# Kernel optimization log

Hardware: AMD Instinct MI355X
Metric: run time of the kernel (lower is better)

Reference implementation:

```python
import jax, jax.numpy as jnp
import numpy as np

CONTEXT = 256   # context_size
INITIAL = 32    # initial_size
HIDDEN = 256    # hidden_size
WINDOW = 64 - 1 # module stores window_size - 1
TEMP = 50000.0  # soft-argmax temperature
MAX_STEPS = CONTEXT - INITIAL  # cur_pt >= 1 guarantees >=1 index advance per step
B = 4096


def setup_inputs() -> dict:
    key = jax.random.key(0)
    ks = jax.random.split(key, 4)
    def lin_w(k, fan_in, fan_out):
        bound = 1.0 / np.sqrt(fan_in)
        return jax.random.uniform(k, (fan_in, fan_out), jnp.float32, -bound, bound)
    return {
        "x": jax.random.normal(ks[0], (B, CONTEXT), jnp.float32),
        "hid_W": lin_w(ks[1], HIDDEN, HIDDEN),
        "hid_b": jnp.zeros((HIDDEN,), jnp.float32),
        "in_W": lin_w(ks[2], INITIAL, HIDDEN),
        "in_b": jnp.zeros((HIDDEN,), jnp.float32),
        "pred_W": lin_w(ks[3], HIDDEN, WINDOW),
        "pred_b": jnp.zeros((WINDOW,), jnp.float32),
    }


def reference(x, hid_W, hid_b, in_W, in_b, pred_W, pred_b):
    # with per-item active masks. Padded/dense outputs:
    #   pts  [B, MAX_STEPS] : predicted change points (last point dropped, rest zero-padded)
    #   mx   [B, CONTEXT]   : all sigmoid-masked slices scattered back to their positions
    # returned concatenated as [B, MAX_STEPS + CONTEXT].
    Bv = x.shape[0]
    rows = jnp.arange(Bv)[:, None]
    jW = jnp.arange(WINDOW, dtype=jnp.float32)
    iI = jnp.arange(INITIAL)
    iWin = jnp.arange(WINDOW)

    def step(carry, _):
        last, hidden, masked_x, count = carry
        active = last < CONTEXT                       # torch: skip items whose last pt >= context
        last_long = last.astype(jnp.int32)            # floor (last >= INITIAL > 0)
        # slice x[i, last-INITIAL : last]; first step last=INITIAL -> x[:, 0:INITIAL]
        idx = last_long[:, None] - INITIAL + iI       # [B, I]
        slices = jnp.take_along_axis(x, idx, axis=1)
        new_hidden = jnp.tanh(hidden @ hid_W + hid_b + slices @ in_W + in_b)
        hidden = jnp.where(active[:, None], new_hidden, hidden)
        w = new_hidden @ pred_W + pred_b              # [B, WINDOW]
        p = jax.nn.softmax(w * TEMP, axis=-1)
        cur_pt = jnp.minimum(p @ jW + 1.0, float(WINDOW))        # soft-argmax + 1, clamped
        seq_end = jnp.minimum(cur_pt + last, float(CONTEXT))
        seq_end_long = seq_end.astype(jnp.int32)
        # masked slice: mask = 1 - sigmoid(j - cur_pt), j in [0, seq_end_long - last_long)
        pos = last_long[:, None] + iWin                            # [B, WINDOW]
        valid = (pos < seq_end_long[:, None]) & active[:, None]
        mask = 1.0 - jax.nn.sigmoid(jW[None, :] - cur_pt[:, None])
        pos_c = jnp.clip(pos, 0, CONTEXT - 1)
        xg = jnp.take_along_axis(x, pos_c, axis=1)
        contrib = jnp.where(valid, mask * xg, 0.0)
        masked_x = masked_x.at[rows, pos_c].add(contrib)           # segments are disjoint
        last = jnp.where(active, seq_end, last)
        count = count + active.astype(jnp.int32)
        return (last, hidden, masked_x, count), jnp.where(active, seq_end, 0.0)

    init = (jnp.full((Bv,), float(INITIAL), jnp.float32),
            jnp.ones((Bv, HIDDEN), jnp.float32),
            jnp.zeros_like(x),
            jnp.zeros((Bv,), jnp.int32))
    (last, hidden, masked_x, count), ys = jax.lax.scan(step, init, None, length=MAX_STEPS)
    pts = ys.T                                                    # [B, MAX_STEPS]
    keep = jnp.arange(MAX_STEPS)[None, :] < (count - 1)[:, None]  # torch drops last pt per item
    pts = jnp.where(keep, pts, 0.0)
    return jnp.concatenate([pts, masked_x], axis=1)               # [B, MAX_STEPS + CONTEXT]
```

## Files before the change

### kernel.cpp

```cpp
#include <hip/hip_runtime.h>
#include <math.h>


#define CTX     256
#define INIT    32
#define HID     256
#define WIN     63
#define MSTEPS  224
#define OUTROW  (MSTEPS + CTX)
#define IT      4
#define NT      256

__global__ void __launch_bounds__(NT, 4)
cpp_kernel(const float* __restrict__ x,
           const float* __restrict__ hid_W,
           const float* __restrict__ hid_b,
           const float* __restrict__ in_W,
           const float* __restrict__ in_b,
           const float* __restrict__ pred_W,
           const float* __restrict__ pred_b,
           float* __restrict__ out)
{
    __shared__ float s_x[IT][CTX];
    __shared__ float s_hid[IT][HID];
    __shared__ int   s_lastl[IT];
    __shared__ int   s_act[IT];

    const int tid  = threadIdx.x;
    const int lane = tid & 63;
    const int q    = tid >> 6;
    const int j    = tid;
    const int item0 = blockIdx.x * IT;

    const double bias  = (double)hid_b[j] + (double)in_b[j];
    const float  pbias = (lane < WIN) ? pred_b[lane] : 0.0f;

    {
        const int item = item0 + q;
        float* orow = out + (size_t)item * OUTROW;
        for (int idx = lane; idx < OUTROW; idx += 64) orow[idx] = 0.0f;
        #pragma unroll
        for (int u = 0; u < 4; ++u)
            s_x[q][lane + 64 * u] = x[(size_t)item * CTX + lane + 64 * u];
        #pragma unroll
        for (int u = 0; u < 4; ++u) s_hid[q][lane + 64 * u] = 1.0f;
        if (lane == 0) { s_lastl[q] = INIT; s_act[q] = 1; }
    }

    float mylast = (float)INIT;
    int   sc = 0;
    __syncthreads();

    for (int iter = 0; iter < MSTEPS; ++iter) {
        int lastl[IT], act[IT];
        #pragma unroll
        for (int it = 0; it < IT; ++it) { lastl[it] = s_lastl[it]; act[it] = s_act[it]; }
        if (!(act[0] | act[1] | act[2] | act[3])) break;

        float ain[IT] = {0.0f, 0.0f, 0.0f, 0.0f};
        {
            int sb[IT];
            #pragma unroll
            for (int it = 0; it < IT; ++it) {
                int l = lastl[it]; if (l > CTX) l = CTX;
                sb[it] = l - INIT;
            }
            #pragma unroll 1
            for (int m = 0; m < INIT; ++m) {
                const float wv = in_W[m * HID + j];
                #pragma unroll
                for (int it = 0; it < IT; ++it)
                    ain[it] = fmaf(s_x[it][sb[it] + m], wv, ain[it]);
            }
        }
        float ah[IT][4];
        #pragma unroll
        for (int it = 0; it < IT; ++it)
            #pragma unroll
            for (int u = 0; u < 4; ++u) ah[it][u] = 0.0f;

        #pragma unroll 1
        for (int k = 0; k < HID; k += 4) {
            const float w0 = hid_W[(size_t)(k + 0) * HID + j];
            const float w1 = hid_W[(size_t)(k + 1) * HID + j];
            const float w2 = hid_W[(size_t)(k + 2) * HID + j];
            const float w3 = hid_W[(size_t)(k + 3) * HID + j];
            #pragma unroll
            for (int it = 0; it < IT; ++it) {
                const float4 h = *(const float4*)&s_hid[it][k];
                ah[it][0] = fmaf(h.x, w0, ah[it][0]);
                ah[it][1] = fmaf(h.y, w1, ah[it][1]);
                ah[it][2] = fmaf(h.z, w2, ah[it][2]);
                ah[it][3] = fmaf(h.w, w3, ah[it][3]);
            }
        }
        __syncthreads();

        #pragma unroll
        for (int it = 0; it < IT; ++it) {
            if (act[it]) {
                const double tot = bias + (double)ain[it]
                                 + (double)ah[it][0] + (double)ah[it][1]
                                 + (double)ah[it][2] + (double)ah[it][3];
                s_hid[it][j] = tanhf((float)tot);
            }
        }
        __syncthreads();

        if (act[q]) {
            const int it = q;
            float t = -INFINITY;
            if (lane < WIN) {
                float b0 = 0.0f, b1 = 0.0f, b2 = 0.0f, b3 = 0.0f;
                #pragma unroll 1
                for (int k = 0; k < HID; k += 4) {
                    const float p0 = pred_W[(k + 0) * WIN + lane];
                    const float p1 = pred_W[(k + 1) * WIN + lane];
                    const float p2 = pred_W[(k + 2) * WIN + lane];
                    const float p3 = pred_W[(k + 3) * WIN + lane];
                    const float4 h = *(const float4*)&s_hid[it][k];
                    b0 = fmaf(h.x, p0, b0);
                    b1 = fmaf(h.y, p1, b1);
                    b2 = fmaf(h.z, p2, b2);
                    b3 = fmaf(h.w, p3, b3);
                }
                const double wv = (double)pbias + (double)b0 + (double)b1
                                + (double)b2 + (double)b3;
                t = (float)wv * 50000.0f;
            }
            float mx = t;
            #pragma unroll
            for (int off = 32; off > 0; off >>= 1)
                mx = fmaxf(mx, __shfl_xor(mx, off));
            const float e = (lane < WIN) ? expf(t - mx) : 0.0f;
            float S = e;
            #pragma unroll
            for (int off = 32; off > 0; off >>= 1)
                S += __shfl_xor(S, off);
            const float p = e / S;
            float D = p * (float)lane;
            #pragma unroll
            for (int off = 32; off > 0; off >>= 1)
                D += __shfl_xor(D, off);
            float cur = fminf(D + 1.0f, 63.0f);
            float se = fminf(cur + mylast, 256.0f);
            const int sel = (int)se;

            float* orow = out + (size_t)(item0 + it) * OUTROW;
            if (lane < WIN) {
                const int pos = lastl[it] + lane;
                if (pos < sel) {
                    const float msk = 1.0f / (1.0f + expf((float)lane - cur));
                    orow[MSTEPS + pos] = msk * s_x[it][pos];
                }
            }
            const bool done = (se >= 256.0f);
            if (lane == 0) {
                if (!done) { orow[sc] = se; s_lastl[it] = sel; }
                else       { s_act[it] = 0; }
            }
            sc++;
            mylast = se;
        }
        __syncthreads();
    }
}

extern "C" void kernel_launch(void* const* d_in, const int* in_sizes, int n_in,
                              void* d_out, int out_size, void* d_ws, size_t ws_size,
                              hipStream_t stream) {
    const float* x      = (const float*)d_in[0];
    const float* hid_W  = (const float*)d_in[1];
    const float* hid_b  = (const float*)d_in[2];
    const float* in_W   = (const float*)d_in[3];
    const float* in_b   = (const float*)d_in[4];
    const float* pred_W = (const float*)d_in[5];
    const float* pred_b = (const float*)d_in[6];
    float* out = (float*)d_out;

    const int B = in_sizes[0] / CTX;
    const int nblocks = B / IT;
    cpp_kernel<<<nblocks, NT, 0, stream>>>(x, hid_W, hid_b, in_W, in_b,
                                           pred_W, pred_b, out);
}
```

Before: 342.5 us.

## Process eight items per block with prefetched weights and two-item prediction per wave

Result: slower. 502.9 us (+46.8%).

```diff
diff --git a/kernel.cpp b/kernel.cpp
--- a/kernel.cpp
+++ b/kernel.cpp
@@ -8,7 +8,7 @@
 #define WIN     63
 #define MSTEPS  224
 #define OUTROW  (MSTEPS + CTX)
-#define IT      4
+#define IT      8
 #define NT      256
 
 __global__ void __launch_bounds__(NT, 4)
@@ -35,29 +35,38 @@
     const double bias  = (double)hid_b[j] + (double)in_b[j];
     const float  pbias = (lane < WIN) ? pred_b[lane] : 0.0f;
 
-    {
-        const int item = item0 + q;
+    #pragma unroll
+    for (int s = 0; s < 2; ++s) {
+        const int it = 2 * q + s;
+        const int item = item0 + it;
         float* orow = out + (size_t)item * OUTROW;
         for (int idx = lane; idx < OUTROW; idx += 64) orow[idx] = 0.0f;
         #pragma unroll
         for (int u = 0; u < 4; ++u)
-            s_x[q][lane + 64 * u] = x[(size_t)item * CTX + lane + 64 * u];
-        #pragma unroll
-        for (int u = 0; u < 4; ++u) s_hid[q][lane + 64 * u] = 1.0f;
-        if (lane == 0) { s_lastl[q] = INIT; s_act[q] = 1; }
+            s_x[it][lane + 64 * u] = x[(size_t)item * CTX + lane + 64 * u];
+        #pragma unroll
+        for (int u = 0; u < 4; ++u) s_hid[it][lane + 64 * u] = 1.0f;
+        if (lane == 0) { s_lastl[it] = INIT; s_act[it] = 1; }
     }
 
-    float mylast = (float)INIT;
-    int   sc = 0;
+    float lastA = (float)INIT, lastB = (float)INIT;
+    int   scA = 0, scB = 0;
     __syncthreads();
 
     for (int iter = 0; iter < MSTEPS; ++iter) {
         int lastl[IT], act[IT];
         #pragma unroll
         for (int it = 0; it < IT; ++it) { lastl[it] = s_lastl[it]; act[it] = s_act[it]; }
-        if (!(act[0] | act[1] | act[2] | act[3])) break;
-
-        float ain[IT] = {0.0f, 0.0f, 0.0f, 0.0f};
+        {
+            int any = 0;
+            #pragma unroll
+            for (int it = 0; it < IT; ++it) any |= act[it];
+            if (!any) break;
+        }
+
+        float ain[IT];
+        #pragma unroll
+        for (int it = 0; it < IT; ++it) ain[it] = 0.0f;
         {
             int sb[IT];
             #pragma unroll
@@ -73,26 +82,41 @@
                     ain[it] = fmaf(s_x[it][sb[it] + m], wv, ain[it]);
             }
         }
-        float ah[IT][4];
-        #pragma unroll
-        for (int it = 0; it < IT; ++it)
-            #pragma unroll
-            for (int u = 0; u < 4; ++u) ah[it][u] = 0.0f;
-
+
+        float c0[IT], c1[IT];
+        #pragma unroll
+        for (int it = 0; it < IT; ++it) { c0[it] = 0.0f; c1[it] = 0.0f; }
+
+        float a0 = hid_W[(size_t)0 * HID + j], a1 = hid_W[(size_t)1 * HID + j];
+        float a2 = hid_W[(size_t)2 * HID + j], a3 = hid_W[(size_t)3 * HID + j];
+        float b0 = hid_W[(size_t)4 * HID + j], b1 = hid_W[(size_t)5 * HID + j];
+        float b2 = hid_W[(size_t)6 * HID + j], b3 = hid_W[(size_t)7 * HID + j];
         #pragma unroll 1
-        for (int k = 0; k < HID; k += 4) {
-            const float w0 = hid_W[(size_t)(k + 0) * HID + j];
-            const float w1 = hid_W[(size_t)(k + 1) * HID + j];
-            const float w2 = hid_W[(size_t)(k + 2) * HID + j];
-            const float w3 = hid_W[(size_t)(k + 3) * HID + j];
+        for (int k = 0; k < HID; k += 8) {
+            const int ka = (k + 8)  & (HID - 1);
+            const float na0 = hid_W[(size_t)(ka + 0) * HID + j];
+            const float na1 = hid_W[(size_t)(ka + 1) * HID + j];
+            const float na2 = hid_W[(size_t)(ka + 2) * HID + j];
+            const float na3 = hid_W[(size_t)(ka + 3) * HID + j];
             #pragma unroll
             for (int it = 0; it < IT; ++it) {
                 const float4 h = *(const float4*)&s_hid[it][k];
-                ah[it][0] = fmaf(h.x, w0, ah[it][0]);
-                ah[it][1] = fmaf(h.y, w1, ah[it][1]);
-                ah[it][2] = fmaf(h.z, w2, ah[it][2]);
-                ah[it][3] = fmaf(h.w, w3, ah[it][3]);
-            }
+                c0[it] = fmaf(h.y, a1, fmaf(h.x, a0, c0[it]));
+                c1[it] = fmaf(h.w, a3, fmaf(h.z, a2, c1[it]));
+            }
+            a0 = na0; a1 = na1; a2 = na2; a3 = na3;
+            const int kb = (k + 12) & (HID - 1);
+            const float nb0 = hid_W[(size_t)(kb + 0) * HID + j];
+            const float nb1 = hid_W[(size_t)(kb + 1) * HID + j];
+            const float nb2 = hid_W[(size_t)(kb + 2) * HID + j];
+            const float nb3 = hid_W[(size_t)(kb + 3) * HID + j];
+            #pragma unroll
+            for (int it = 0; it < IT; ++it) {
+                const float4 h = *(const float4*)&s_hid[it][k + 4];
+                c0[it] = fmaf(h.y, b1, fmaf(h.x, b0, c0[it]));
+                c1[it] = fmaf(h.w, b3, fmaf(h.z, b2, c1[it]));
+            }
+            b0 = nb0; b1 = nb1; b2 = nb2; b3 = nb3;
         }
         __syncthreads();
 
@@ -100,34 +124,39 @@
         for (int it = 0; it < IT; ++it) {
             if (act[it]) {
                 const double tot = bias + (double)ain[it]
-                                 + (double)ah[it][0] + (double)ah[it][1]
-                                 + (double)ah[it][2] + (double)ah[it][3];
+                                 + (double)c0[it] + (double)c1[it];
                 s_hid[it][j] = tanhf((float)tot);
             }
         }
         __syncthreads();
 
-        if (act[q]) {
-            const int it = q;
-            float t = -INFINITY;
-            if (lane < WIN) {
-                float b0 = 0.0f, b1 = 0.0f, b2 = 0.0f, b3 = 0.0f;
-                #pragma unroll 1
-                for (int k = 0; k < HID; k += 4) {
-                    const float p0 = pred_W[(k + 0) * WIN + lane];
-                    const float p1 = pred_W[(k + 1) * WIN + lane];
-                    const float p2 = pred_W[(k + 2) * WIN + lane];
-                    const float p3 = pred_W[(k + 3) * WIN + lane];
-                    const float4 h = *(const float4*)&s_hid[it][k];
-                    b0 = fmaf(h.x, p0, b0);
-                    b1 = fmaf(h.y, p1, b1);
-                    b2 = fmaf(h.z, p2, b2);
-                    b3 = fmaf(h.w, p3, b3);
-                }
-                const double wv = (double)pbias + (double)b0 + (double)b1
-                                + (double)b2 + (double)b3;
-                t = (float)wv * 50000.0f;
-            }
+        const int itA = 2 * q, itB = 2 * q + 1;
+        float tA = -INFINITY, tB = -INFINITY;
+        if (lane < WIN && (act[itA] | act[itB])) {
+            float pA0 = 0.0f, pA1 = 0.0f, pB0 = 0.0f, pB1 = 0.0f;
+            float g0 = pred_W[0 * WIN + lane], g1 = pred_W[1 * WIN + lane];
+            float g2 = pred_W[2 * WIN + lane], g3 = pred_W[3 * WIN + lane];
+            #pragma unroll 1
+            for (int k = 0; k < HID; k += 4) {
+                const int kn = (k + 4) & (HID - 1);
+                const float n0 = pred_W[(kn + 0) * WIN + lane];
+                const float n1 = pred_W[(kn + 1) * WIN + lane];
+                const float n2 = pred_W[(kn + 2) * WIN + lane];
+                const float n3 = pred_W[(kn + 3) * WIN + lane];
+                const float4 hA = *(const float4*)&s_hid[itA][k];
+                const float4 hB = *(const float4*)&s_hid[itB][k];
+                pA0 = fmaf(hA.y, g1, fmaf(hA.x, g0, pA0));
+                pA1 = fmaf(hA.w, g3, fmaf(hA.z, g2, pA1));
+                pB0 = fmaf(hB.y, g1, fmaf(hB.x, g0, pB0));
+                pB1 = fmaf(hB.w, g3, fmaf(hB.z, g2, pB1));
+                g0 = n0; g1 = n1; g2 = n2; g3 = n3;
+            }
+            tA = (float)((double)pbias + (double)pA0 + (double)pA1) * 50000.0f;
+            tB = (float)((double)pbias + (double)pB0 + (double)pB1) * 50000.0f;
+        }
+
+        auto phaseC = [&](int it, float t, float& mylast, int& sc) {
+            if (!act[it]) return;
             float mx = t;
             #pragma unroll
             for (int off = 32; off > 0; off >>= 1)
@@ -161,7 +190,10 @@
             }
             sc++;
             mylast = se;
-        }
+        };
+        phaseC(itA, tA, lastA, scA);
+        phaseC(itB, tB, lastB, scB);
+
         __syncthreads();
     }
 }
```
